# Kernel optimization log

Hardware: AMD Instinct MI355X
Metric: run time of the kernel (lower is better)

## Reference

```python
import jax, jax.numpy as jnp
import numpy as np

EMBED = 256
NUM_DEPTH = 128
NUM_CAMS = 1


def _bilinear_sample(img, x, y):
    # img: [H, W, E]; x, y: [L] pixel coords (align_corners=False, zero padding)
    H, W, _ = img.shape
    x0f = jnp.floor(x); y0f = jnp.floor(y)
    ix0 = x0f.astype(jnp.int32); iy0 = y0f.astype(jnp.int32)
    ix1 = ix0 + 1; iy1 = iy0 + 1
    wx1 = x - x0f; wx0 = 1.0 - wx1
    wy1 = y - y0f; wy0 = 1.0 - wy1

    def g(iy, ix):
        valid = (ix >= 0) & (ix < W) & (iy >= 0) & (iy < H)
        v = img[jnp.clip(iy, 0, H - 1), jnp.clip(ix, 0, W - 1)]  # [L, E]
        return jnp.where(valid[:, None], v, jnp.zeros((), img.dtype))

    return (g(iy0, ix0) * (wy0 * wx0)[:, None] + g(iy0, ix1) * (wy0 * wx1)[:, None]
            + g(iy1, ix0) * (wy1 * wx0)[:, None] + g(iy1, ix1) * (wy1 * wx1)[:, None])


def setup_inputs() -> dict:
    rng = jax.random.key(0)
    ks = jax.random.split(rng, 7)
    H = W = 64
    nv = H * W           # num_value == num_query (forced by output*key broadcast)
    bsv = 1
    return {
        "query": jax.random.normal(ks[0], (bsv, nv, EMBED), jnp.float32),
        "key": jax.random.normal(ks[1], (NUM_CAMS, nv, bsv, EMBED), jnp.float32),
        "value": jax.random.normal(ks[2], (NUM_CAMS, nv, bsv, EMBED), jnp.float32),
        "identity": jax.random.normal(ks[3], (bsv, nv, NUM_DEPTH), jnp.float32),
        "ref_3d": jax.random.uniform(ks[4], (bsv * NUM_CAMS, nv * NUM_DEPTH, 2), jnp.float32),
        "spatial_shapes": jnp.array([[H, W]], jnp.int32),
        "W_attn": jax.random.normal(ks[5], (NUM_CAMS * NUM_DEPTH, EMBED), jnp.float32) * 0.02,
        "b_attn": jax.random.normal(ks[6], (NUM_CAMS * NUM_DEPTH,), jnp.float32) * 0.02,
    }


def reference(query, key, value, identity, ref_3d, spatial_shapes, W_attn, b_attn):
    bsv, num_query, _ = query.shape
    num_cams, num_value, bs, _ = key.shape
    H = int(spatial_shapes[0, 0]); W = int(spatial_shapes[0, 1])

    # key/value rearrange (value flipped over cams dim, a no-op for num_cams=1)
    key_r = jnp.transpose(key, (2, 0, 1, 3)).reshape(bsv, num_value, EMBED)
    val_r = jnp.transpose(value[::-1], (2, 0, 1, 3)).reshape(bsv * num_cams, num_value, EMBED)

    # attention weights: Linear -> softmax over (levels*points)=1 axis (== ones)
    aw = query @ W_attn.T + b_attn                               # [bsv, nq, cams*depth]
    aw = aw.reshape(bsv, num_query, num_cams, NUM_DEPTH, 1, 1)    # heads=1, lv*pt=1
    aw = jax.nn.softmax(aw, axis=-1)
    aw = jnp.transpose(aw.reshape(bsv, num_query, num_cams, NUM_DEPTH, 1, 1, 1),
                       (0, 2, 1, 3, 4, 5, 6))
    aw = aw.reshape(bsv * num_cams, num_query * NUM_DEPTH)        # [B, L]

    # deformable bilinear sampling (single level/head/point)
    grids = 2.0 * ref_3d - 1.0                                   # grid_sample convention
    px = ((grids[..., 0] + 1.0) * W - 1.0) / 2.0                  # [B, L]
    py = ((grids[..., 1] + 1.0) * H - 1.0) / 2.0
    imgs = val_r.reshape(bsv * num_cams, H, W, EMBED)
    sampled = jax.vmap(_bilinear_sample)(imgs, px, py)            # [B, L, E]

    out = sampled * aw[:, :, None]                                # weighted gather
    out = out.reshape(bsv, num_cams, num_query, NUM_DEPTH, EMBED).mean(axis=1)

    # elementwise dot with key features, scaled
    out = jnp.sum(out * key_r[:, :, None, :], axis=-1) / jnp.sqrt(jnp.float32(EMBED))
    return out + identity                                         # [bsv, nq, num_depth]
```

## Files before the change

### kernel.cpp

```cpp
#include <hip/hip_runtime.h>

#define EMBED 256
#define NUM_DEPTH 128

typedef __attribute__((ext_vector_type(8))) short bf16x8;
typedef __attribute__((ext_vector_type(4))) float f32x4;

__device__ __forceinline__ unsigned short f2b(float f) {
    union { float f; unsigned u; } c; c.f = f;
    unsigned u = c.u;
    u += 0x7fffu + ((u >> 16) & 1u);
    return (unsigned short)(u >> 16);
}
__device__ __forceinline__ float b2f(unsigned short h) {
    union { unsigned u; float f; } c; c.u = ((unsigned)h) << 16;
    return c.f;
}

__global__ __launch_bounds__(256) void cvt_kernel(
    const float4* __restrict__ key, const float4* __restrict__ val,
    ushort4* __restrict__ kb, ushort4* __restrict__ vb, int n4)
{
    int i = blockIdx.x * blockDim.x + threadIdx.x;
    if (i >= n4) return;
    float4 a = key[i];
    float4 b = val[i];
    kb[i] = make_ushort4(f2b(a.x), f2b(a.y), f2b(a.z), f2b(a.w));
    vb[i] = make_ushort4(f2b(b.x), f2b(b.y), f2b(b.z), f2b(b.w));
}

__global__ __launch_bounds__(256) void gemm_nt_bf16(
    const unsigned short* __restrict__ A,
    const unsigned short* __restrict__ B,
    unsigned short* __restrict__ D,
    int N)
{
    __shared__ __align__(16) unsigned short As[128 * 32];
    __shared__ __align__(16) unsigned short Bs[128 * 32];

    const int m0 = blockIdx.y * 128;
    const int n0 = blockIdx.x * 128;
    const int tid  = threadIdx.x;
    const int lane = tid & 63;
    const int wave = tid >> 6;
    const int wm = (wave & 1) * 64;
    const int wn = (wave >> 1) * 64;

    f32x4 acc[4][4] = {};

    const int srow = lane >> 2;
    const int scol = (lane & 3) * 8;
    const int k8 = (lane >> 4) * 8;
    const int fm = lane & 15;

    for (int kt = 0; kt < EMBED; kt += 32) {
        #pragma unroll
        for (int t = 0; t < 2; ++t) {
            const int c = wave * 2 + t;
            const int row = c * 16 + srow;
            const unsigned short* ga = A + (size_t)(m0 + row) * EMBED + kt + scol;
            const unsigned short* gb = B + (size_t)(n0 + row) * EMBED + kt + scol;
            __builtin_amdgcn_global_load_lds(
                (const __attribute__((address_space(1))) void*)ga,
                (__attribute__((address_space(3))) void*)(As + c * 512), 16, 0, 0);
            __builtin_amdgcn_global_load_lds(
                (const __attribute__((address_space(1))) void*)gb,
                (__attribute__((address_space(3))) void*)(Bs + c * 512), 16, 0, 0);
        }
        __syncthreads();

        bf16x8 af[4], bfr[4];
        #pragma unroll
        for (int i = 0; i < 4; ++i) {
            af[i]  = *(const bf16x8*)(As + (wm + i * 16 + fm) * 32 + k8);
            bfr[i] = *(const bf16x8*)(Bs + (wn + i * 16 + fm) * 32 + k8);
        }
        #pragma unroll
        for (int i = 0; i < 4; ++i)
            #pragma unroll
            for (int j = 0; j < 4; ++j)
                acc[i][j] = __builtin_amdgcn_mfma_f32_16x16x32_bf16(af[i], bfr[j], acc[i][j], 0, 0, 0);
        __syncthreads();
    }

    const int col = lane & 15;
    const int rbase = (lane >> 4) * 4;
    #pragma unroll
    for (int i = 0; i < 4; ++i) {
        #pragma unroll
        for (int j = 0; j < 4; ++j) {
            const int m = m0 + wm + i * 16 + rbase;
            const int n = n0 + wn + j * 16 + col;
            #pragma unroll
            for (int r = 0; r < 4; ++r)
                D[(size_t)(m + r) * N + n] = f2b(acc[i][j][r]);
        }
    }
}

__global__ __launch_bounds__(256) void gather_kernel(
    const unsigned short* __restrict__ D,
    const float* __restrict__ identity,
    const float* __restrict__ ref3d,
    const int*   __restrict__ spatial,
    float* __restrict__ out, int total, int nv)
{
    int l = blockIdx.x * blockDim.x + threadIdx.x;
    if (l >= total) return;
    const int Hs = spatial[0], Ws = spatial[1];
    const int q = l >> 7;

    const float2 r2 = reinterpret_cast<const float2*>(ref3d)[l];
    const float px = r2.x * (float)Ws - 0.5f;
    const float py = r2.y * (float)Hs - 0.5f;
    const float x0f = floorf(px), y0f = floorf(py);
    const int ix0 = (int)x0f, iy0 = (int)y0f;
    const int ix1 = ix0 + 1,  iy1 = iy0 + 1;
    const float wx1 = px - x0f, wx0 = 1.0f - wx1;
    const float wy1 = py - y0f, wy0 = 1.0f - wy1;
    const bool vx0 = (ix0 >= 0) & (ix0 < Ws);
    const bool vx1 = (ix1 >= 0) & (ix1 < Ws);

    const unsigned short* row = D + (size_t)q * nv;
    float acc = 0.f;
    if (iy0 >= 0 && iy0 < Hs) {
        if (vx0) acc = fmaf(wy0 * wx0, b2f(row[iy0 * Ws + ix0]), acc);
        if (vx1) acc = fmaf(wy0 * wx1, b2f(row[iy0 * Ws + ix1]), acc);
    }
    if (iy1 >= 0 && iy1 < Hs) {
        if (vx0) acc = fmaf(wy1 * wx0, b2f(row[iy1 * Ws + ix0]), acc);
        if (vx1) acc = fmaf(wy1 * wx1, b2f(row[iy1 * Ws + ix1]), acc);
    }
    out[l] = fmaf(acc, 0.0625f, identity[l]);
}

__global__ __launch_bounds__(256) void uv_direct_kernel(
    const float* __restrict__ key, const float* __restrict__ value,
    const float* __restrict__ identity, const float* __restrict__ ref3d,
    const int* __restrict__ spatial, float* __restrict__ out)
{
    const int q = blockIdx.x;
    const int tid = threadIdx.x;
    const int lane = tid & 63;
    const int wave = tid >> 6;
    const int H = spatial[0], W = spatial[1];
    const int row4 = EMBED / 4;
    const float4 k4 = reinterpret_cast<const float4*>(key + (size_t)q * EMBED)[lane];
    const float4* __restrict__ v4 = reinterpret_cast<const float4*>(value);
    for (int d = wave; d < NUM_DEPTH; d += 4) {
        const int l = q * NUM_DEPTH + d;
        const float rx = ref3d[2 * l], ry = ref3d[2 * l + 1];
        const float px = rx * (float)W - 0.5f, py = ry * (float)H - 0.5f;
        const float x0f = floorf(px), y0f = floorf(py);
        const int ix0 = (int)x0f, iy0 = (int)y0f, ix1 = ix0 + 1, iy1 = iy0 + 1;
        const float wx1 = px - x0f, wx0 = 1.f - wx1, wy1 = py - y0f, wy0 = 1.f - wy1;
        float4 acc = make_float4(0.f, 0.f, 0.f, 0.f);
        #define TAP(IY, IX, WGT) \
            if ((IY) >= 0 && (IY) < H && (IX) >= 0 && (IX) < W) { \
                const float w_ = (WGT); \
                const float4 t = v4[(size_t)((IY) * W + (IX)) * row4 + lane]; \
                acc.x = fmaf(w_, t.x, acc.x); acc.y = fmaf(w_, t.y, acc.y); \
                acc.z = fmaf(w_, t.z, acc.z); acc.w = fmaf(w_, t.w, acc.w); }
        TAP(iy0, ix0, wy0 * wx0) TAP(iy0, ix1, wy0 * wx1)
        TAP(iy1, ix0, wy1 * wx0) TAP(iy1, ix1, wy1 * wx1)
        #undef TAP
        float partial = acc.x * k4.x + acc.y * k4.y + acc.z * k4.z + acc.w * k4.w;
        #pragma unroll
        for (int off = 32; off > 0; off >>= 1) partial += __shfl_xor(partial, off, 64);
        if (lane == 0) out[l] = fmaf(partial, 0.0625f, identity[l]);
    }
}

extern "C" void kernel_launch(void* const* d_in, const int* in_sizes, int n_in,
                              void* d_out, int out_size, void* d_ws, size_t ws_size,
                              hipStream_t stream) {
    const float* key      = (const float*)d_in[1];
    const float* value    = (const float*)d_in[2];
    const float* identity = (const float*)d_in[3];
    const float* ref3d    = (const float*)d_in[4];
    const int*   spatial  = (const int*)d_in[5];
    float* out = (float*)d_out;

    const int nq = in_sizes[3] / NUM_DEPTH;
    const int nv = in_sizes[1] / EMBED;
    const int total = nq * NUM_DEPTH;

    const size_t d_bytes  = (size_t)nq * nv * sizeof(unsigned short);
    const size_t kb_bytes = (size_t)nq * EMBED * sizeof(unsigned short);
    const size_t vb_bytes = (size_t)nv * EMBED * sizeof(unsigned short);
    const size_t need = d_bytes + kb_bytes + vb_bytes;

    if (ws_size < need || (nq % 128) || (nv % 128)) {
        uv_direct_kernel<<<nq, 256, 0, stream>>>(key, value, identity, ref3d, spatial, out);
        return;
    }

    unsigned short* D  = (unsigned short*)d_ws;
    unsigned short* kb = (unsigned short*)((char*)d_ws + d_bytes);
    unsigned short* vb = (unsigned short*)((char*)d_ws + d_bytes + kb_bytes);

    const int n4 = nq * EMBED / 4;
    cvt_kernel<<<(n4 + 255) / 256, 256, 0, stream>>>(
        (const float4*)key, (const float4*)value, (ushort4*)kb, (ushort4*)vb, n4);

    dim3 grid(nv / 128, nq / 128);
    gemm_nt_bf16<<<grid, 256, 0, stream>>>(kb, vb, D, nv);

    gather_kernel<<<(total + 255) / 256, 256, 0, stream>>>(
        D, identity, ref3d, spatial, out, total, nv);
}
```

Measured before the change: 104.7 us.

## Fuse GEMM with bilinear gather via per-query row binning and LDS tile

```diff
diff --git a/kernel.cpp b/kernel.cpp
--- a/kernel.cpp
+++ b/kernel.cpp
@@ -29,17 +29,66 @@
     vb[i] = make_ushort4(f2b(b.x), f2b(b.y), f2b(b.z), f2b(b.w));
 }
 
-__global__ __launch_bounds__(256) void gemm_nt_bf16(
+__global__ __launch_bounds__(128) void bin_kernel(
+    const float* __restrict__ ref3d, const float* __restrict__ identity,
+    const int* __restrict__ spatial,
+    unsigned char* __restrict__ dlist, unsigned short* __restrict__ offs,
+    int offs_stride, float2* __restrict__ pxy, float* __restrict__ out)
+{
+    const int q = blockIdx.x;
+    const int d = threadIdx.x;
+    const int H = spatial[0], W = spatial[1];
+    const int l = q * NUM_DEPTH + d;
+
+    const float2 r2 = reinterpret_cast<const float2*>(ref3d)[l];
+    const float px = r2.x * (float)W - 0.5f;
+    const float py = r2.y * (float)H - 0.5f;
+    const int iy0 = (int)floorf(py);
+    const int b = min(max(iy0, -1), H) + 1;
+
+    __shared__ unsigned int cnt[132];
+    __shared__ unsigned int base[132];
+    for (int i = d; i < H + 2; i += NUM_DEPTH) cnt[i] = 0;
+    __syncthreads();
+    const unsigned pos_in_bin = atomicAdd(&cnt[b], 1u);
+    __syncthreads();
+    if (d == 0) {
+        unsigned s = 0;
+        for (int i = 0; i < H + 2; ++i) { base[i] = s; s += cnt[i]; }
+        base[H + 2] = s;
+    }
+    __syncthreads();
+    for (int i = d; i < H + 3; i += NUM_DEPTH)
+        offs[(size_t)q * offs_stride + i] = (unsigned short)base[i];
+    const unsigned pos = base[b] + pos_in_bin;
+    dlist[(size_t)q * NUM_DEPTH + pos] = (unsigned char)d;
+    pxy[(size_t)q * NUM_DEPTH + pos] = make_float2(px, py);
+    out[l] = identity[l];
+}
+
+__global__ __launch_bounds__(256) void fused_kernel(
     const unsigned short* __restrict__ A,
     const unsigned short* __restrict__ B,
-    unsigned short* __restrict__ D,
-    int N)
+    const unsigned char* __restrict__ dlist,
+    const unsigned short* __restrict__ offs, int offs_stride,
+    const float2* __restrict__ pxy,
+    const int* __restrict__ spatial,
+    float* __restrict__ out)
 {
     __shared__ __align__(16) unsigned short As[128 * 32];
     __shared__ __align__(16) unsigned short Bs[128 * 32];
-
+    __shared__ __align__(16) unsigned short Dt[128 * 128];
+    __shared__ unsigned int scanbuf[128];
+    __shared__ unsigned int qpref[129];
+    __shared__ unsigned int qstart[128];
+
+    const int H = spatial[0], W = spatial[1];
+    const int Rt = 128 / W;
     const int m0 = blockIdx.y * 128;
-    const int n0 = blockIdx.x * 128;
+    const int jt = blockIdx.x;
+    const int n0 = jt * 128;
+    const int iy_lo = Rt * jt;
+
     const int tid  = threadIdx.x;
     const int lane = tid & 63;
     const int wave = tid >> 6;
@@ -83,55 +132,73 @@
         __syncthreads();
     }
 
+    unsigned my_s = 0, my_e = 0;
+    if (tid < 128) {
+        const size_t ob = (size_t)(m0 + tid) * offs_stride;
+        my_s = offs[ob + Rt * jt];
+        my_e = offs[ob + Rt * jt + Rt + 1];
+    }
+
     const int col = lane & 15;
     const int rbase = (lane >> 4) * 4;
     #pragma unroll
-    for (int i = 0; i < 4; ++i) {
+    for (int i = 0; i < 4; ++i)
         #pragma unroll
         for (int j = 0; j < 4; ++j) {
-            const int m = m0 + wm + i * 16 + rbase;
-            const int n = n0 + wn + j * 16 + col;
+            const int rr = wm + i * 16 + rbase;
+            const int cc = wn + j * 16 + col;
             #pragma unroll
             for (int r = 0; r < 4; ++r)
-                D[(size_t)(m + r) * N + n] = f2b(acc[i][j][r]);
-        }
-    }
-}
-
-__global__ __launch_bounds__(256) void gather_kernel(
-    const unsigned short* __restrict__ D,
-    const float* __restrict__ identity,
-    const float* __restrict__ ref3d,
-    const int*   __restrict__ spatial,
-    float* __restrict__ out, int total, int nv)
-{
-    int l = blockIdx.x * blockDim.x + threadIdx.x;
-    if (l >= total) return;
-    const int Hs = spatial[0], Ws = spatial[1];
-    const int q = l >> 7;
-
-    const float2 r2 = reinterpret_cast<const float2*>(ref3d)[l];
-    const float px = r2.x * (float)Ws - 0.5f;
-    const float py = r2.y * (float)Hs - 0.5f;
-    const float x0f = floorf(px), y0f = floorf(py);
-    const int ix0 = (int)x0f, iy0 = (int)y0f;
-    const int ix1 = ix0 + 1,  iy1 = iy0 + 1;
-    const float wx1 = px - x0f, wx0 = 1.0f - wx1;
-    const float wy1 = py - y0f, wy0 = 1.0f - wy1;
-    const bool vx0 = (ix0 >= 0) & (ix0 < Ws);
-    const bool vx1 = (ix1 >= 0) & (ix1 < Ws);
-
-    const unsigned short* row = D + (size_t)q * nv;
-    float acc = 0.f;
-    if (iy0 >= 0 && iy0 < Hs) {
-        if (vx0) acc = fmaf(wy0 * wx0, b2f(row[iy0 * Ws + ix0]), acc);
-        if (vx1) acc = fmaf(wy0 * wx1, b2f(row[iy0 * Ws + ix1]), acc);
-    }
-    if (iy1 >= 0 && iy1 < Hs) {
-        if (vx0) acc = fmaf(wy1 * wx0, b2f(row[iy1 * Ws + ix0]), acc);
-        if (vx1) acc = fmaf(wy1 * wx1, b2f(row[iy1 * Ws + ix1]), acc);
-    }
-    out[l] = fmaf(acc, 0.0625f, identity[l]);
+                Dt[(rr + r) * 128 + cc] = f2b(acc[i][j][r]);
+        }
+
+    if (tid < 128) { qstart[tid] = my_s; scanbuf[tid] = my_e - my_s; }
+    __syncthreads();
+
+    #pragma unroll
+    for (int off = 1; off < 128; off <<= 1) {
+        unsigned v = (tid < 128 && tid >= off) ? scanbuf[tid - off] : 0u;
+        __syncthreads();
+        if (tid < 128) scanbuf[tid] += v;
+        __syncthreads();
+    }
+    if (tid < 128) qpref[tid + 1] = scanbuf[tid];
+    if (tid == 0) qpref[0] = 0;
+    __syncthreads();
+
+    const unsigned T = qpref[128];
+    for (unsigned e = tid; e < T; e += 256) {
+        int lo = 0, hi = 127;
+        while (lo < hi) {
+            const int mid = (lo + hi + 1) >> 1;
+            if (qpref[mid] <= e) lo = mid; else hi = mid - 1;
+        }
+        const int q = lo;
+        const unsigned pos = qstart[q] + (e - qpref[q]);
+        const size_t rowb = (size_t)(m0 + q) * NUM_DEPTH;
+        const int d = dlist[rowb + pos];
+        const float2 c2 = pxy[rowb + pos];
+        const float px = c2.x, py = c2.y;
+        const float x0f = floorf(px), y0f = floorf(py);
+        const int ix0 = (int)x0f, iy0 = (int)y0f;
+        const float wx1 = px - x0f, wx0 = 1.0f - wx1;
+        const float wy1 = py - y0f, wy0 = 1.0f - wy1;
+
+        float accv = 0.f;
+        bool hit = false;
+        #pragma unroll
+        for (int ky = 0; ky < 2; ++ky) {
+            const int iy = iy0 + ky;
+            if (iy < iy_lo || iy >= iy_lo + Rt) continue;
+            const float wy = ky ? wy1 : wy0;
+            const int base_p = q * 128 + (iy - iy_lo) * W;
+            if (ix0 >= 0 && ix0 < W) { accv = fmaf(wy * wx0, b2f(Dt[base_p + ix0]), accv); hit = true; }
+            const int ix1 = ix0 + 1;
+            if (ix1 >= 0 && ix1 < W) { accv = fmaf(wy * wx1, b2f(Dt[base_p + ix1]), accv); hit = true; }
+        }
+        if (hit)
+            atomicAdd(&out[(size_t)(m0 + q) * NUM_DEPTH + d], accv * 0.0625f);
+    }
 }
 
 __global__ __launch_bounds__(256) void uv_direct_kernel(
@@ -183,29 +250,35 @@
 
     const int nq = in_sizes[3] / NUM_DEPTH;
     const int nv = in_sizes[1] / EMBED;
-    const int total = nq * NUM_DEPTH;
-
-    const size_t d_bytes  = (size_t)nq * nv * sizeof(unsigned short);
-    const size_t kb_bytes = (size_t)nq * EMBED * sizeof(unsigned short);
-    const size_t vb_bytes = (size_t)nv * EMBED * sizeof(unsigned short);
-    const size_t need = d_bytes + kb_bytes + vb_bytes;
+    const int OFFS_STRIDE = 131;
+
+    const size_t kb_b   = ((size_t)nq * EMBED * 2 + 255) & ~(size_t)255;
+    const size_t vb_b   = ((size_t)nv * EMBED * 2 + 255) & ~(size_t)255;
+    const size_t dl_b   = ((size_t)nq * NUM_DEPTH + 255) & ~(size_t)255;
+    const size_t of_b   = ((size_t)nq * OFFS_STRIDE * 2 + 255) & ~(size_t)255;
+    const size_t px_b   = ((size_t)nq * NUM_DEPTH * 8 + 255) & ~(size_t)255;
+    const size_t need = kb_b + vb_b + dl_b + of_b + px_b;
 
     if (ws_size < need || (nq % 128) || (nv % 128)) {
         uv_direct_kernel<<<nq, 256, 0, stream>>>(key, value, identity, ref3d, spatial, out);
         return;
     }
 
-    unsigned short* D  = (unsigned short*)d_ws;
-    unsigned short* kb = (unsigned short*)((char*)d_ws + d_bytes);
-    unsigned short* vb = (unsigned short*)((char*)d_ws + d_bytes + kb_bytes);
+    char* p = (char*)d_ws;
+    unsigned short* kb   = (unsigned short*)p;           p += kb_b;
+    unsigned short* vb   = (unsigned short*)p;           p += vb_b;
+    unsigned char*  dlist= (unsigned char*)p;            p += dl_b;
+    unsigned short* offs = (unsigned short*)p;           p += of_b;
+    float2*         pxy  = (float2*)p;
 
     const int n4 = nq * EMBED / 4;
     cvt_kernel<<<(n4 + 255) / 256, 256, 0, stream>>>(
         (const float4*)key, (const float4*)value, (ushort4*)kb, (ushort4*)vb, n4);
 
+    bin_kernel<<<nq, NUM_DEPTH, 0, stream>>>(
+        ref3d, identity, spatial, dlist, offs, OFFS_STRIDE, pxy, out);
+
     dim3 grid(nv / 128, nq / 128);
-    gemm_nt_bf16<<<grid, 256, 0, stream>>>(kb, vb, D, nv);
-
-    gather_kernel<<<(total + 255) / 256, 256, 0, stream>>>(
-        D, identity, ref3d, spatial, out, total, nv);
-}
+    fused_kernel<<<grid, 256, 0, stream>>>(
+        kb, vb, dlist, offs, OFFS_STRIDE, pxy, spatial, out);
+}
```

Result: slower. 128.4 us (+22.7%).

## Stage GEMM epilogue through LDS and gather from LDS-staged score rows

Applied to the files above, without the earlier changes.

```diff
diff --git a/kernel.cpp b/kernel.cpp
--- a/kernel.cpp
+++ b/kernel.cpp
@@ -2,6 +2,7 @@
 
 #define EMBED 256
 #define NUM_DEPTH 128
+#define CT_STRIDE 136
 
 typedef __attribute__((ext_vector_type(8))) short bf16x8;
 typedef __attribute__((ext_vector_type(4))) float f32x4;
@@ -35,8 +36,9 @@
     unsigned short* __restrict__ D,
     int N)
 {
-    __shared__ __align__(16) unsigned short As[128 * 32];
-    __shared__ __align__(16) unsigned short Bs[128 * 32];
+    __shared__ __align__(16) unsigned short Ct[128 * CT_STRIDE];
+    unsigned short* As = Ct;
+    unsigned short* Bs = Ct + 128 * 32;
 
     const int m0 = blockIdx.y * 128;
     const int n0 = blockIdx.x * 128;
@@ -86,15 +88,23 @@
     const int col = lane & 15;
     const int rbase = (lane >> 4) * 4;
     #pragma unroll
-    for (int i = 0; i < 4; ++i) {
+    for (int i = 0; i < 4; ++i)
         #pragma unroll
         for (int j = 0; j < 4; ++j) {
-            const int m = m0 + wm + i * 16 + rbase;
-            const int n = n0 + wn + j * 16 + col;
+            const int rr = wm + i * 16 + rbase;
+            const int cc = wn + j * 16 + col;
             #pragma unroll
             for (int r = 0; r < 4; ++r)
-                D[(size_t)(m + r) * N + n] = f2b(acc[i][j][r]);
+                Ct[(rr + r) * CT_STRIDE + cc] = f2b(acc[i][j][r]);
         }
+    __syncthreads();
+
+    #pragma unroll
+    for (int it = 0; it < 8; ++it) {
+        const int r  = it * 16 + (tid >> 4);
+        const int c8 = (tid & 15) * 8;
+        const int4 v = *(const int4*)(Ct + r * CT_STRIDE + c8);
+        *(int4*)(D + (size_t)(m0 + r) * N + n0 + c8) = v;
     }
 }
 
@@ -103,12 +113,22 @@
     const float* __restrict__ identity,
     const float* __restrict__ ref3d,
     const int*   __restrict__ spatial,
-    float* __restrict__ out, int total, int nv)
-{
-    int l = blockIdx.x * blockDim.x + threadIdx.x;
-    if (l >= total) return;
+    float* __restrict__ out, int nv)
+{
+    __shared__ unsigned short Ds[2 * 4096];
+
+    const int q0 = blockIdx.x * 2;
+    const int tid = threadIdx.x;
+
+    const int4* src = (const int4*)(D + (size_t)q0 * nv);
+    int4* dst = (int4*)Ds;
+    const int nchunk = (2 * nv) / 8;
+    for (int i = tid; i < nchunk; i += 256) dst[i] = src[i];
+    __syncthreads();
+
     const int Hs = spatial[0], Ws = spatial[1];
-    const int q = l >> 7;
+    const int l = q0 * NUM_DEPTH + tid;
+    const int qi = tid >> 7;
 
     const float2 r2 = reinterpret_cast<const float2*>(ref3d)[l];
     const float px = r2.x * (float)Ws - 0.5f;
@@ -121,7 +141,7 @@
     const bool vx0 = (ix0 >= 0) & (ix0 < Ws);
     const bool vx1 = (ix1 >= 0) & (ix1 < Ws);
 
-    const unsigned short* row = D + (size_t)q * nv;
+    const unsigned short* row = Ds + qi * nv;
     float acc = 0.f;
     if (iy0 >= 0 && iy0 < Hs) {
         if (vx0) acc = fmaf(wy0 * wx0, b2f(row[iy0 * Ws + ix0]), acc);
@@ -183,14 +203,13 @@
 
     const int nq = in_sizes[3] / NUM_DEPTH;
     const int nv = in_sizes[1] / EMBED;
-    const int total = nq * NUM_DEPTH;
 
     const size_t d_bytes  = (size_t)nq * nv * sizeof(unsigned short);
     const size_t kb_bytes = (size_t)nq * EMBED * sizeof(unsigned short);
     const size_t vb_bytes = (size_t)nv * EMBED * sizeof(unsigned short);
     const size_t need = d_bytes + kb_bytes + vb_bytes;
 
-    if (ws_size < need || (nq % 128) || (nv % 128)) {
+    if (ws_size < need || (nq % 128) || (nv % 128) || nv > 4096 || (nq % 2)) {
         uv_direct_kernel<<<nq, 256, 0, stream>>>(key, value, identity, ref3d, spatial, out);
         return;
     }
@@ -206,6 +225,5 @@
     dim3 grid(nv / 128, nq / 128);
     gemm_nt_bf16<<<grid, 256, 0, stream>>>(kb, vb, D, nv);
 
-    gather_kernel<<<(total + 255) / 256, 256, 0, stream>>>(
-        D, identity, ref3d, spatial, out, total, nv);
-}
+    gather_kernel<<<nq / 2, 256, 0, stream>>>(D, identity, ref3d, spatial, out, nv);
+}
```

Result: faster. 99.00 us (-5.4%).
